# Kernel optimization log

Hardware: AMD Instinct MI355X
Metric: run time of the kernel (lower is better)

The kernel has to match this reference:

```python
import jax, jax.numpy as jnp
import numpy as np

T = 0.07  # temperature from __init__ default


def setup_inputs() -> dict:
    key = jax.random.key(0)
    ks = jax.random.split(key, 5)
    B, D, H, E = 4096, 2048, 2048, 128
    init = lambda k, shp, fan: jax.random.normal(k, shp, dtype=jnp.float32) * (1.0 / np.sqrt(fan))
    return {
        "input1": jax.random.normal(ks[0], (B, D), dtype=jnp.float32),
        "input2": jax.random.normal(ks[1], (B, D), dtype=jnp.float32),
        "W0": init(ks[2], (D, H), D), "b0": jnp.zeros((H,), jnp.float32),
        "W1": init(ks[3], (H, H), H), "b1": jnp.zeros((H,), jnp.float32),
        "W2": init(ks[4], (H, E), H), "b2": jnp.zeros((E,), jnp.float32),
    }


def _mlp(x, W0, b0, W1, b1, W2, b2):
    # Linear -> ReLU -> Linear -> Linear (ReLU only between hidden layers)
    x = jax.nn.relu(x @ W0 + b0)
    x = x @ W1 + b1
    return x @ W2 + b2


def reference(input1, input2, W0, b0, W1, b1, W2, b2):
    B = input1.shape[0]
    e1 = _mlp(input1, W0, b0, W1, b1, W2, b2)
    e2 = _mlp(input2, W0, b0, W1, b1, W2, b2)
    feats = jnp.stack([e1, e2], axis=1)                       # [B, 2, E]
    feats = feats / jnp.linalg.norm(feats, axis=2, keepdims=True)
    # view(N,2,dim).permute(1,0,2).reshape(2N,dim): view0 rows then view1 rows
    f = jnp.concatenate([feats[:, 0], feats[:, 1]], axis=0)   # [2B, E]
    N2 = 2 * B
    sim = (f @ f.T) / T                                        # [2B, 2B]
    idx = jnp.arange(N2)
    pos = sim[idx, (idx + B) % N2]                             # partner view similarity
    # exclude self-similarity (diagonal) from the logsumexp denominator
    sim = jnp.where(jnp.eye(N2, dtype=bool), jnp.float32(-1e9), sim)
    # CE with positive at index 0 of [pos, negatives] == -pos + logsumexp(non-self)
    loss = jnp.mean(jax.nn.logsumexp(sim, axis=1) - pos)
    return loss
```

## Files before the change

kernel.cpp:

```cpp
#include <hip/hip_runtime.h>
#include <stdint.h>

typedef float f32x4 __attribute__((ext_vector_type(4)));
typedef float f32x16 __attribute__((ext_vector_type(16)));
typedef __bf16 bf16x8 __attribute__((ext_vector_type(8)));
typedef unsigned short u16;
typedef unsigned int u32;

#define INVT 14.285714285714286f

__device__ __forceinline__ u16 f2bf(float f) {
  u32 u = __float_as_uint(f);
  u32 r = (u + 0x7fffu + ((u >> 16) & 1u)) >> 16;
  return (u16)r;
}
__device__ __forceinline__ float bf2f(u16 h) { return __uint_as_float(((u32)h) << 16); }

__device__ __forceinline__ void g2l16(const void* g, void* l) {
  auto gp = reinterpret_cast<__attribute__((address_space(1))) uint32_t*>(
      reinterpret_cast<uintptr_t>(g));
  auto lp = reinterpret_cast<__attribute__((address_space(3))) uint32_t*>(
      reinterpret_cast<uintptr_t>(l));
  __builtin_amdgcn_global_load_lds(gp, lp, 16, 0, 0);
}

__global__ __launch_bounds__(256) void k_cvt2(const float* __restrict__ in1,
                                              const float* __restrict__ in2,
                                              u16* __restrict__ out) {
  int i = (blockIdx.x * 256 + threadIdx.x) * 4;
  float4 v;
  if (i < 8388608) v = *(const float4*)(in1 + i);
  else             v = *(const float4*)(in2 + (i - 8388608));
  ushort4 p;
  p.x = f2bf(v.x); p.y = f2bf(v.y); p.z = f2bf(v.z); p.w = f2bf(v.w);
  *(ushort4*)(out + i) = p;
}

__global__ __launch_bounds__(256) void k_transpose2(const float* __restrict__ w0,
                                                    u16* __restrict__ w0t,
                                                    const float* __restrict__ w1,
                                                    u16* __restrict__ w1t) {
  const float* in = blockIdx.z ? w1 : w0;
  u16* out = blockIdx.z ? w1t : w0t;
  const int R = 2048, C = 2048;
  __shared__ float t[64][65];
  const int r0 = blockIdx.y * 64, c0 = blockIdx.x * 64;
#pragma unroll
  for (int p = 0; p < 16; ++p) {
    int idx = p * 256 + threadIdx.x;
    int r = idx >> 6, c = idx & 63;
    t[r][c] = in[(size_t)(r0 + r) * C + (c0 + c)];
  }
  __syncthreads();
#pragma unroll
  for (int p = 0; p < 16; ++p) {
    int idx = p * 256 + threadIdx.x;
    int c = idx >> 6, r = idx & 63;
    out[(size_t)(c0 + c) * R + (r0 + r)] = f2bf(t[r][c]);
  }
}

__global__ __launch_bounds__(256) void k_transpose(const float* __restrict__ in,
                                                   u16* __restrict__ out, int R, int C) {
  __shared__ float t[64][65];
  const int r0 = blockIdx.y * 64, c0 = blockIdx.x * 64;
#pragma unroll
  for (int p = 0; p < 16; ++p) {
    int idx = p * 256 + threadIdx.x;
    int r = idx >> 6, c = idx & 63;
    t[r][c] = in[(size_t)(r0 + r) * C + (c0 + c)];
  }
  __syncthreads();
#pragma unroll
  for (int p = 0; p < 16; ++p) {
    int idx = p * 256 + threadIdx.x;
    int c = idx >> 6, r = idx & 63;
    out[(size_t)(c0 + c) * R + (r0 + r)] = f2bf(t[r][c]);
  }
}

__global__ __launch_bounds__(256, 4) void k_gemm(const u16* __restrict__ A, const u16* __restrict__ Bt,
                                                 const float* __restrict__ bias, u16* __restrict__ C,
                                                 int M, int N, int K, int relu) {
  __shared__ __align__(16) u16 sm[16384];
  const int tid = threadIdx.x;
  const int l = tid & 63, w = tid >> 6;
  const int wm = w >> 1, wn = w & 1;

  const int flat = blockIdx.y * gridDim.x + blockIdx.x;
  const int xcd = flat & 7, slot = flat >> 3;
  const int nb = xcd * 2 + (slot >> 6), mb = slot & 63;
  const int m0 = mb * 128, n0 = nb * 128;

  const int rs = w * 16 + (l >> 2);
  const int kb = ((l & 3) ^ ((rs >> 1) & 3)) * 16;
  const char* gA = (const char*)(A + (size_t)(m0 + rs) * K) + kb;
  const char* gB = (const char*)(Bt + (size_t)(n0 + rs) * K) + kb;
  const size_t radv = (size_t)64 * K * 2;
  char* lbase = (char*)sm + w * 1024 + l * 16;

  auto issue = [&](int kc, int b) {
    char* d = lbase + b * 16384;
    g2l16(gA + kc, d);
    g2l16(gA + radv + kc, d + 4096);
    g2l16(gB + kc, d + 8192);
    g2l16(gB + radv + kc, d + 12288);
  };

  const int rA = wm * 64 + (l & 31);
  const int rB = wn * 64 + (l & 31);
  const int c0 = l >> 5;
  const int sA = (rA >> 1) & 3, sB = (rB >> 1) & 3;

  f32x16 acc[2][2] = {};

  auto compute = [&](int b) {
    const u16* As = sm + b * 8192;
    const u16* Bs = As + 4096;
    bf16x8 af[2][2], bfr[2][2];
#pragma unroll
    for (int t = 0; t < 2; ++t) {
      const int ca = (((t << 1) + c0) ^ sA) * 8;
      const int cb = (((t << 1) + c0) ^ sB) * 8;
#pragma unroll
      for (int fm = 0; fm < 2; ++fm) af[t][fm] = *(const bf16x8*)(As + (rA + fm * 32) * 32 + ca);
#pragma unroll
      for (int fn = 0; fn < 2; ++fn) bfr[t][fn] = *(const bf16x8*)(Bs + (rB + fn * 32) * 32 + cb);
    }
#pragma unroll
    for (int t = 0; t < 2; ++t)
#pragma unroll
      for (int fm = 0; fm < 2; ++fm)
#pragma unroll
        for (int fn = 0; fn < 2; ++fn)
          acc[fm][fn] = __builtin_amdgcn_mfma_f32_32x32x16_bf16(af[t][fm], bfr[t][fn],
                                                                acc[fm][fn], 0, 0, 0);
  };

#define PHASE(BCUR, BNEXT)                                            \
  {                                                                   \
    if (k + 32 < K) {                                                 \
      issue((k + 32) * 2, BNEXT);                                     \
      asm volatile("s_waitcnt vmcnt(4)\ns_barrier" ::: "memory");     \
    } else {                                                          \
      asm volatile("s_waitcnt vmcnt(0)\ns_barrier" ::: "memory");     \
    }                                                                 \
    compute(BCUR);                                                    \
    asm volatile("s_barrier" ::: "memory");                           \
    k += 32;                                                          \
  }

  issue(0, 0);
  int k = 0;
  do { PHASE(0, 1) PHASE(1, 0) } while (k < K);
#undef PHASE

  const int colb = n0 + wn * 64 + (l & 31);
  const int rowb = m0 + wm * 64 + 4 * (l >> 5);
#pragma unroll
  for (int fn = 0; fn < 2; ++fn) {
    const float b = bias[colb + fn * 32];
#pragma unroll
    for (int fm = 0; fm < 2; ++fm)
#pragma unroll
      for (int g = 0; g < 4; ++g)
#pragma unroll
        for (int rr = 0; rr < 4; ++rr) {
          float v = acc[fm][fn][g * 4 + rr] + b;
          if (relu) v = fmaxf(v, 0.0f);
          C[(size_t)(rowb + fm * 32 + g * 8 + rr) * N + colb + fn * 32] = f2bf(v);
        }
  }
}

__global__ __launch_bounds__(256, 4) void k_gemm_sk(const u16* __restrict__ A, const u16* __restrict__ Bt,
                                                    float* __restrict__ Ep, int K, int Ksplit) {
  __shared__ __align__(16) u16 sm[16384];
  const int tid = threadIdx.x;
  const int l = tid & 63, w = tid >> 6;
  const int wm = w >> 1, wn = w & 1;
  const int m0 = blockIdx.y * 128;
  const int split = blockIdx.x;
  const int k0s = split * Ksplit;

  const int rs = w * 16 + (l >> 2);
  const int kb = ((l & 3) ^ ((rs >> 1) & 3)) * 16;
  const char* gA = (const char*)(A + (size_t)(m0 + rs) * K + k0s) + kb;
  const char* gB = (const char*)(Bt + (size_t)rs * K + k0s) + kb;
  const size_t radv = (size_t)64 * K * 2;
  char* lbase = (char*)sm + w * 1024 + l * 16;

  auto issue = [&](int kc, int b) {
    char* d = lbase + b * 16384;
    g2l16(gA + kc, d);
    g2l16(gA + radv + kc, d + 4096);
    g2l16(gB + kc, d + 8192);
    g2l16(gB + radv + kc, d + 12288);
  };

  const int rA = wm * 64 + (l & 31);
  const int rB = wn * 64 + (l & 31);
  const int c0 = l >> 5;
  const int sA = (rA >> 1) & 3, sB = (rB >> 1) & 3;

  f32x16 acc[2][2] = {};

  auto compute = [&](int b) {
    const u16* As = sm + b * 8192;
    const u16* Bs = As + 4096;
    bf16x8 af[2][2], bfr[2][2];
#pragma unroll
    for (int t = 0; t < 2; ++t) {
      const int ca = (((t << 1) + c0) ^ sA) * 8;
      const int cb = (((t << 1) + c0) ^ sB) * 8;
#pragma unroll
      for (int fm = 0; fm < 2; ++fm) af[t][fm] = *(const bf16x8*)(As + (rA + fm * 32) * 32 + ca);
#pragma unroll
      for (int fn = 0; fn < 2; ++fn) bfr[t][fn] = *(const bf16x8*)(Bs + (rB + fn * 32) * 32 + cb);
    }
#pragma unroll
    for (int t = 0; t < 2; ++t)
#pragma unroll
      for (int fm = 0; fm < 2; ++fm)
#pragma unroll
        for (int fn = 0; fn < 2; ++fn)
          acc[fm][fn] = __builtin_amdgcn_mfma_f32_32x32x16_bf16(af[t][fm], bfr[t][fn],
                                                                acc[fm][fn], 0, 0, 0);
  };

#define PHASE(BCUR, BNEXT)                                            \
  {                                                                   \
    if (k + 32 < Ksplit) {                                            \
      issue((k + 32) * 2, BNEXT);                                     \
      asm volatile("s_waitcnt vmcnt(4)\ns_barrier" ::: "memory");     \
    } else {                                                          \
      asm volatile("s_waitcnt vmcnt(0)\ns_barrier" ::: "memory");     \
    }                                                                 \
    compute(BCUR);                                                    \
    asm volatile("s_barrier" ::: "memory");                           \
    k += 32;                                                          \
  }

  issue(0, 0);
  int k = 0;
  do { PHASE(0, 1) PHASE(1, 0) } while (k < Ksplit);
#undef PHASE

  const int colb = wn * 64 + (l & 31);
  const int rowb = wm * 64 + 4 * (l >> 5);
#pragma unroll
  for (int fn = 0; fn < 2; ++fn)
#pragma unroll
    for (int fm = 0; fm < 2; ++fm)
#pragma unroll
      for (int g = 0; g < 4; ++g)
#pragma unroll
        for (int rr = 0; rr < 4; ++rr)
          Ep[((size_t)split * 8192 + m0 + rowb + fm * 32 + g * 8 + rr) * 128 + colb + fn * 32] =
              acc[fm][fn][g * 4 + rr];
}

__global__ __launch_bounds__(256) void k_norm(const float* __restrict__ Ep,
                                              const float* __restrict__ b2, u16* __restrict__ F) {
  const int l = threadIdx.x & 63, w = threadIdx.x >> 6;
  const int row = blockIdx.x * 4 + w;
  const float2* base = (const float2*)Ep + (size_t)row * 64 + l;
  float x = 0.f, y = 0.f;
#pragma unroll
  for (int s = 0; s < 4; ++s) {
    float2 t = base[(size_t)s * (8192 * 64)];
    x += t.x; y += t.y;
  }
  x += b2[l * 2]; y += b2[l * 2 + 1];
  float sq = x * x + y * y;
#pragma unroll
  for (int off = 1; off < 64; off <<= 1) sq += __shfl_xor(sq, off);
  const float inv = 1.0f / sqrtf(sq);
  F[(size_t)row * 128 + l * 2] = f2bf(x * inv);
  F[(size_t)row * 128 + l * 2 + 1] = f2bf(y * inv);
}

__global__ __launch_bounds__(256) void k_sim(const u16* __restrict__ F, float* __restrict__ Sp) {
  __shared__ __align__(16) u16 As[64 * 128];
  const int tid = threadIdx.x;
  const int l = tid & 63, w = tid >> 6;
  const int wm = w >> 1, wn = w & 1;
  const int row0 = blockIdx.y * 64;
  const int chunk = blockIdx.x;

#pragma unroll
  for (int j = 0; j < 4; ++j) {
    const int c = j * 4 + w;
    const int r = c * 4 + (l >> 4);
    const int cb = (l & 15) * 16;
    g2l16((const char*)(F + (size_t)(row0 + r) * 128) + cb, (char*)As + c * 1024 + l * 16);
  }
  asm volatile("s_waitcnt vmcnt(0)" ::: "memory");
  __syncthreads();

  bf16x8 af[2][4];
#pragma unroll
  for (int i = 0; i < 2; ++i)
#pragma unroll
    for (int s = 0; s < 4; ++s)
      af[i][s] = *(const bf16x8*)(As + (wm * 32 + i * 16 + (l & 15)) * 128 + s * 32 + (l >> 4) * 8);

  float runS[2][4] = {};
#pragma unroll 1
  for (int ct = 0; ct < 16; ++ct) {
    const int n0 = chunk * 2048 + ct * 128 + wn * 64;
    f32x4 acc[2][4] = {};
#pragma unroll
    for (int j = 0; j < 4; ++j) {
      const u16* bp = F + (size_t)(n0 + j * 16 + (l & 15)) * 128 + (l >> 4) * 8;
#pragma unroll
      for (int s = 0; s < 4; ++s) {
        bf16x8 bfr = *(const bf16x8*)(bp + s * 32);
        acc[0][j] = __builtin_amdgcn_mfma_f32_16x16x32_bf16(af[0][s], bfr, acc[0][j], 0, 0, 0);
        acc[1][j] = __builtin_amdgcn_mfma_f32_16x16x32_bf16(af[1][s], bfr, acc[1][j], 0, 0, 0);
      }
    }
#pragma unroll
    for (int i = 0; i < 2; ++i) {
      const int rb = row0 + wm * 32 + i * 16 + ((l >> 4) << 2);
#pragma unroll
      for (int r = 0; r < 4; ++r) {
        const int grow = rb + r;
        float sp = 0.f;
#pragma unroll
        for (int j = 0; j < 4; ++j) {
          const int gcol = n0 + j * 16 + (l & 15);
          float v = acc[i][j][r] * INVT;
          v = (gcol == grow) ? -1e30f : v;
          sp += __expf(v - INVT);
        }
        sp += __shfl_xor(sp, 1);
        sp += __shfl_xor(sp, 2);
        sp += __shfl_xor(sp, 4);
        sp += __shfl_xor(sp, 8);
        runS[i][r] += sp;
      }
    }
  }

  __syncthreads();
  float* red = (float*)As;
  if (wn == 0 && (l & 15) == 0) {
#pragma unroll
    for (int i = 0; i < 2; ++i)
#pragma unroll
      for (int r = 0; r < 4; ++r)
        red[wm * 32 + i * 16 + ((l >> 4) << 2) + r] = runS[i][r];
  }
  __syncthreads();
  if (wn == 1 && (l & 15) == 0) {
#pragma unroll
    for (int i = 0; i < 2; ++i)
#pragma unroll
      for (int r = 0; r < 4; ++r) {
        const int rr = wm * 32 + i * 16 + ((l >> 4) << 2) + r;
        Sp[(size_t)chunk * 8192 + row0 + rr] = red[rr] + runS[i][r];
      }
  }
}

__global__ __launch_bounds__(256) void k_combine(const float* __restrict__ Sp,
                                                 const u16* __restrict__ F,
                                                 float* __restrict__ out) {
  const int r = blockIdx.x * 256 + threadIdx.x;
  float S = Sp[r] + Sp[8192 + r] + Sp[2 * 8192 + r] + Sp[3 * 8192 + r];
  const float lse = INVT + logf(S);
  const int par = (r + 4096) & 8191;
  const u16* a = F + (size_t)r * 128;
  const u16* b = F + (size_t)par * 128;
  float dot = 0.f;
#pragma unroll 8
  for (int k = 0; k < 128; ++k) dot = fmaf(bf2f(a[k]), bf2f(b[k]), dot);
  float contrib = lse - dot * INVT;
#pragma unroll
  for (int off = 1; off < 64; off <<= 1) contrib += __shfl_xor(contrib, off);
  if ((threadIdx.x & 63) == 0) atomicAdd(out, contrib * (1.0f / 8192.0f));
}

extern "C" void kernel_launch(void* const* d_in, const int* in_sizes, int n_in,
                              void* d_out, int out_size, void* d_ws, size_t ws_size,
                              hipStream_t stream) {
  const float* input1 = (const float*)d_in[0];
  const float* input2 = (const float*)d_in[1];
  const float* W0 = (const float*)d_in[2];
  const float* b0 = (const float*)d_in[3];
  const float* W1 = (const float*)d_in[4];
  const float* b1 = (const float*)d_in[5];
  const float* W2 = (const float*)d_in[6];
  const float* b2 = (const float*)d_in[7];
  float* out = (float*)d_out;
  char* ws = (char*)d_ws;

  u16* Xb = (u16*)(ws + 0);
  u16* H1 = (u16*)(ws + 33554432);
  u16* W0T = (u16*)(ws + 67108864);
  u16* W1T = (u16*)(ws + 75497472);
  float* Ep = (float*)(ws + 67108864);
  u16* W2T = (u16*)(ws + 83886080);
  u16* Ff = (u16*)(ws + 84410368);
  float* Sp = (float*)(ws + 86507520);
  u16* H2 = Xb;

  hipMemsetAsync(d_out, 0, sizeof(float), stream);
  k_cvt2<<<16384, 256, 0, stream>>>(input1, input2, Xb);
  k_transpose2<<<dim3(32, 32, 2), 256, 0, stream>>>(W0, W0T, W1, W1T);
  k_transpose<<<dim3(2, 32), 256, 0, stream>>>(W2, W2T, 2048, 128);
  k_gemm<<<dim3(16, 64), 256, 0, stream>>>(Xb, W0T, b0, H1, 8192, 2048, 2048, 1);
  k_gemm<<<dim3(16, 64), 256, 0, stream>>>(H1, W1T, b1, H2, 8192, 2048, 2048, 0);
  k_gemm_sk<<<dim3(4, 64), 256, 0, stream>>>(H2, W2T, Ep, 2048, 512);
  k_norm<<<2048, 256, 0, stream>>>(Ep, b2, Ff);
  k_sim<<<dim3(4, 128), 256, 0, stream>>>(Ff, Sp);
  k_combine<<<32, 256, 0, stream>>>(Sp, Ff, out);
}
```

Before: 403.4 us.

## Enlarge GEMM tiles to 256x128 with triple-buffered LDS pipeline

The main GEMMs now use 256x128 block tiles, giving each wave 4x2 MFMA accumulators instead of 2x2 and halving the grid. Both GEMM kernels switch from double buffering with two barriers per k-step to a three-stage LDS ring with one barrier per step, issuing loads two tiles ahead. The larger tiles raise operand reuse per LDS load and cut global traffic per FLOP. In exchange, LDS and register use rise, occupancy drops to two blocks per CU, and the XCD-aware block remapping is removed.

Result: faster. 374.6 us (-7.1%).

```diff
diff --git a/kernel.cpp b/kernel.cpp
--- a/kernel.cpp
+++ b/kernel.cpp
@@ -79,89 +79,81 @@
   }
 }
 
-__global__ __launch_bounds__(256, 4) void k_gemm(const u16* __restrict__ A, const u16* __restrict__ Bt,
+__global__ __launch_bounds__(256, 2) void k_gemm(const u16* __restrict__ A, const u16* __restrict__ Bt,
                                                  const float* __restrict__ bias, u16* __restrict__ C,
                                                  int M, int N, int K, int relu) {
-  __shared__ __align__(16) u16 sm[16384];
+  __shared__ __align__(16) u16 sm[36864];
   const int tid = threadIdx.x;
   const int l = tid & 63, w = tid >> 6;
   const int wm = w >> 1, wn = w & 1;
-
-  const int flat = blockIdx.y * gridDim.x + blockIdx.x;
-  const int xcd = flat & 7, slot = flat >> 3;
-  const int nb = xcd * 2 + (slot >> 6), mb = slot & 63;
-  const int m0 = mb * 128, n0 = nb * 128;
-
-  const int rs = w * 16 + (l >> 2);
-  const int kb = ((l & 3) ^ ((rs >> 1) & 3)) * 16;
-  const char* gA = (const char*)(A + (size_t)(m0 + rs) * K) + kb;
-  const char* gB = (const char*)(Bt + (size_t)(n0 + rs) * K) + kb;
-  const size_t radv = (size_t)64 * K * 2;
-  char* lbase = (char*)sm + w * 1024 + l * 16;
-
-  auto issue = [&](int kc, int b) {
-    char* d = lbase + b * 16384;
-    g2l16(gA + kc, d);
-    g2l16(gA + radv + kc, d + 4096);
-    g2l16(gB + kc, d + 8192);
-    g2l16(gB + radv + kc, d + 12288);
+  const int m0 = blockIdx.y * 256, n0 = blockIdx.x * 128;
+
+  const int kb = ((l & 3) ^ ((l >> 3) & 3)) * 16;
+  const char* gA = (const char*)(A + (size_t)(m0 + w * 64 + (l >> 2)) * K) + kb;
+  const char* gB = (const char*)(Bt + (size_t)(n0 + w * 32 + (l >> 2)) * K) + kb;
+  const size_t chRows = (size_t)16 * K * 2;
+
+  auto issue = [&](int kcB, int stg) {
+    char* base = (char*)sm + stg * 24576;
+    char* dA = base + (w * 4) * 1024 + l * 16;
+    char* dB = base + 16384 + (w * 2) * 1024 + l * 16;
+#pragma unroll
+    for (int j = 0; j < 4; ++j) g2l16(gA + j * chRows + kcB, dA + j * 1024);
+#pragma unroll
+    for (int j = 0; j < 2; ++j) g2l16(gB + j * chRows + kcB, dB + j * 1024);
   };
 
-  const int rA = wm * 64 + (l & 31);
-  const int rB = wn * 64 + (l & 31);
+  const int lm = l & 31;
   const int c0 = l >> 5;
-  const int sA = (rA >> 1) & 3, sB = (rB >> 1) & 3;
-
-  f32x16 acc[2][2] = {};
-
-  auto compute = [&](int b) {
-    const u16* As = sm + b * 8192;
-    const u16* Bs = As + 4096;
-    bf16x8 af[2][2], bfr[2][2];
+  const int sw = (lm >> 1) & 3;
+
+  f32x16 acc[4][2] = {};
+
+  auto compute = [&](int stg) {
+    const u16* As = sm + stg * 12288;
+    const u16* Bs = As + 8192;
 #pragma unroll
     for (int t = 0; t < 2; ++t) {
-      const int ca = (((t << 1) + c0) ^ sA) * 8;
-      const int cb = (((t << 1) + c0) ^ sB) * 8;
-#pragma unroll
-      for (int fm = 0; fm < 2; ++fm) af[t][fm] = *(const bf16x8*)(As + (rA + fm * 32) * 32 + ca);
-#pragma unroll
-      for (int fn = 0; fn < 2; ++fn) bfr[t][fn] = *(const bf16x8*)(Bs + (rB + fn * 32) * 32 + cb);
-    }
-#pragma unroll
-    for (int t = 0; t < 2; ++t)
-#pragma unroll
-      for (int fm = 0; fm < 2; ++fm)
+      const int cc = (((t << 1) + c0) ^ sw) * 8;
+      bf16x8 a4[4], b2[2];
+#pragma unroll
+      for (int fm = 0; fm < 4; ++fm)
+        a4[fm] = *(const bf16x8*)(As + (wm * 128 + fm * 32 + lm) * 32 + cc);
+#pragma unroll
+      for (int fn = 0; fn < 2; ++fn)
+        b2[fn] = *(const bf16x8*)(Bs + (wn * 64 + fn * 32 + lm) * 32 + cc);
+#pragma unroll
+      for (int fm = 0; fm < 4; ++fm)
 #pragma unroll
         for (int fn = 0; fn < 2; ++fn)
-          acc[fm][fn] = __builtin_amdgcn_mfma_f32_32x32x16_bf16(af[t][fm], bfr[t][fn],
+          acc[fm][fn] = __builtin_amdgcn_mfma_f32_32x32x16_bf16(a4[fm], b2[fn],
                                                                 acc[fm][fn], 0, 0, 0);
+    }
   };
 
-#define PHASE(BCUR, BNEXT)                                            \
-  {                                                                   \
-    if (k + 32 < K) {                                                 \
-      issue((k + 32) * 2, BNEXT);                                     \
-      asm volatile("s_waitcnt vmcnt(4)\ns_barrier" ::: "memory");     \
-    } else {                                                          \
-      asm volatile("s_waitcnt vmcnt(0)\ns_barrier" ::: "memory");     \
-    }                                                                 \
-    compute(BCUR);                                                    \
-    asm volatile("s_barrier" ::: "memory");                           \
-    k += 32;                                                          \
-  }
-
+  const int NK = K >> 5;
   issue(0, 0);
-  int k = 0;
-  do { PHASE(0, 1) PHASE(1, 0) } while (k < K);
-#undef PHASE
-
-  const int colb = n0 + wn * 64 + (l & 31);
-  const int rowb = m0 + wm * 64 + 4 * (l >> 5);
+  issue(64, 1);
+  int st = 0;
+  for (int kt = 0; kt < NK; ++kt) {
+    if (kt + 1 < NK) asm volatile("s_waitcnt vmcnt(6)" ::: "memory");
+    else             asm volatile("s_waitcnt vmcnt(0)" ::: "memory");
+    asm volatile("s_barrier" ::: "memory");
+    if (kt + 2 < NK) {
+      int stp = st + 2; if (stp >= 3) stp -= 3;
+      issue((kt + 2) * 64, stp);
+    }
+    compute(st);
+    ++st; if (st == 3) st = 0;
+  }
+
+  const int colb = n0 + wn * 64 + lm;
+  const int rowb = m0 + wm * 128 + 4 * c0;
 #pragma unroll
   for (int fn = 0; fn < 2; ++fn) {
     const float b = bias[colb + fn * 32];
 #pragma unroll
-    for (int fm = 0; fm < 2; ++fm)
+    for (int fm = 0; fm < 4; ++fm)
 #pragma unroll
       for (int g = 0; g < 4; ++g)
 #pragma unroll
@@ -173,9 +165,9 @@
   }
 }
 
-__global__ __launch_bounds__(256, 4) void k_gemm_sk(const u16* __restrict__ A, const u16* __restrict__ Bt,
+__global__ __launch_bounds__(256, 2) void k_gemm_sk(const u16* __restrict__ A, const u16* __restrict__ Bt,
                                                     float* __restrict__ Ep, int K, int Ksplit) {
-  __shared__ __align__(16) u16 sm[16384];
+  __shared__ __align__(16) u16 sm[24576];
   const int tid = threadIdx.x;
   const int l = tid & 63, w = tid >> 6;
   const int wm = w >> 1, wn = w & 1;
@@ -183,71 +175,65 @@
   const int split = blockIdx.x;
   const int k0s = split * Ksplit;
 
-  const int rs = w * 16 + (l >> 2);
-  const int kb = ((l & 3) ^ ((rs >> 1) & 3)) * 16;
-  const char* gA = (const char*)(A + (size_t)(m0 + rs) * K + k0s) + kb;
-  const char* gB = (const char*)(Bt + (size_t)rs * K + k0s) + kb;
+  const int kb = ((l & 3) ^ ((l >> 3) & 3)) * 16;
+  const char* gA = (const char*)(A + (size_t)(m0 + w * 16 + (l >> 2)) * K + k0s) + kb;
+  const char* gB = (const char*)(Bt + (size_t)(w * 16 + (l >> 2)) * K + k0s) + kb;
   const size_t radv = (size_t)64 * K * 2;
-  char* lbase = (char*)sm + w * 1024 + l * 16;
-
-  auto issue = [&](int kc, int b) {
-    char* d = lbase + b * 16384;
-    g2l16(gA + kc, d);
-    g2l16(gA + radv + kc, d + 4096);
-    g2l16(gB + kc, d + 8192);
-    g2l16(gB + radv + kc, d + 12288);
+
+  auto issue = [&](int kcB, int stg) {
+    char* base = (char*)sm + stg * 16384;
+    char* dA = base + w * 1024 + l * 16;
+    char* dB = base + 8192 + w * 1024 + l * 16;
+    g2l16(gA + kcB, dA);
+    g2l16(gA + radv + kcB, dA + 4096);
+    g2l16(gB + kcB, dB);
+    g2l16(gB + radv + kcB, dB + 4096);
   };
 
-  const int rA = wm * 64 + (l & 31);
-  const int rB = wn * 64 + (l & 31);
+  const int lm = l & 31;
   const int c0 = l >> 5;
-  const int sA = (rA >> 1) & 3, sB = (rB >> 1) & 3;
+  const int sw = (lm >> 1) & 3;
 
   f32x16 acc[2][2] = {};
 
-  auto compute = [&](int b) {
-    const u16* As = sm + b * 8192;
+  auto compute = [&](int stg) {
+    const u16* As = sm + stg * 8192;
     const u16* Bs = As + 4096;
-    bf16x8 af[2][2], bfr[2][2];
 #pragma unroll
     for (int t = 0; t < 2; ++t) {
-      const int ca = (((t << 1) + c0) ^ sA) * 8;
-      const int cb = (((t << 1) + c0) ^ sB) * 8;
-#pragma unroll
-      for (int fm = 0; fm < 2; ++fm) af[t][fm] = *(const bf16x8*)(As + (rA + fm * 32) * 32 + ca);
-#pragma unroll
-      for (int fn = 0; fn < 2; ++fn) bfr[t][fn] = *(const bf16x8*)(Bs + (rB + fn * 32) * 32 + cb);
-    }
-#pragma unroll
-    for (int t = 0; t < 2; ++t)
+      const int cc = (((t << 1) + c0) ^ sw) * 8;
+      bf16x8 a2[2], b2[2];
+#pragma unroll
+      for (int fm = 0; fm < 2; ++fm) a2[fm] = *(const bf16x8*)(As + (wm * 64 + fm * 32 + lm) * 32 + cc);
+#pragma unroll
+      for (int fn = 0; fn < 2; ++fn) b2[fn] = *(const bf16x8*)(Bs + (wn * 64 + fn * 32 + lm) * 32 + cc);
 #pragma unroll
       for (int fm = 0; fm < 2; ++fm)
 #pragma unroll
         for (int fn = 0; fn < 2; ++fn)
-          acc[fm][fn] = __builtin_amdgcn_mfma_f32_32x32x16_bf16(af[t][fm], bfr[t][fn],
+          acc[fm][fn] = __builtin_amdgcn_mfma_f32_32x32x16_bf16(a2[fm], b2[fn],
                                                                 acc[fm][fn], 0, 0, 0);
+    }
   };
 
-#define PHASE(BCUR, BNEXT)                                            \
-  {                                                                   \
-    if (k + 32 < Ksplit) {                                            \
-      issue((k + 32) * 2, BNEXT);                                     \
-      asm volatile("s_waitcnt vmcnt(4)\ns_barrier" ::: "memory");     \
-    } else {                                                          \
-      asm volatile("s_waitcnt vmcnt(0)\ns_barrier" ::: "memory");     \
-    }                                                                 \
-    compute(BCUR);                                                    \
-    asm volatile("s_barrier" ::: "memory");                           \
-    k += 32;                                                          \
-  }
-
+  const int NK = Ksplit >> 5;
   issue(0, 0);
-  int k = 0;
-  do { PHASE(0, 1) PHASE(1, 0) } while (k < Ksplit);
-#undef PHASE
-
-  const int colb = wn * 64 + (l & 31);
-  const int rowb = wm * 64 + 4 * (l >> 5);
+  issue(64, 1);
+  int st = 0;
+  for (int kt = 0; kt < NK; ++kt) {
+    if (kt + 1 < NK) asm volatile("s_waitcnt vmcnt(4)" ::: "memory");
+    else             asm volatile("s_waitcnt vmcnt(0)" ::: "memory");
+    asm volatile("s_barrier" ::: "memory");
+    if (kt + 2 < NK) {
+      int stp = st + 2; if (stp >= 3) stp -= 3;
+      issue((kt + 2) * 64, stp);
+    }
+    compute(st);
+    ++st; if (st == 3) st = 0;
+  }
+
+  const int colb = wn * 64 + lm;
+  const int rowb = m0 + wm * 64 + 4 * c0;
 #pragma unroll
   for (int fn = 0; fn < 2; ++fn)
 #pragma unroll
@@ -256,7 +242,7 @@
       for (int g = 0; g < 4; ++g)
 #pragma unroll
         for (int rr = 0; rr < 4; ++rr)
-          Ep[((size_t)split * 8192 + m0 + rowb + fm * 32 + g * 8 + rr) * 128 + colb + fn * 32] =
+          Ep[((size_t)split * 8192 + rowb + fm * 32 + g * 8 + rr) * 128 + colb + fn * 32] =
               acc[fm][fn][g * 4 + rr];
 }
 
@@ -410,8 +396,8 @@
   k_cvt2<<<16384, 256, 0, stream>>>(input1, input2, Xb);
   k_transpose2<<<dim3(32, 32, 2), 256, 0, stream>>>(W0, W0T, W1, W1T);
   k_transpose<<<dim3(2, 32), 256, 0, stream>>>(W2, W2T, 2048, 128);
-  k_gemm<<<dim3(16, 64), 256, 0, stream>>>(Xb, W0T, b0, H1, 8192, 2048, 2048, 1);
-  k_gemm<<<dim3(16, 64), 256, 0, stream>>>(H1, W1T, b1, H2, 8192, 2048, 2048, 0);
+  k_gemm<<<dim3(16, 32), 256, 0, stream>>>(Xb, W0T, b0, H1, 8192, 2048, 2048, 1);
+  k_gemm<<<dim3(16, 32), 256, 0, stream>>>(H1, W1T, b1, H2, 8192, 2048, 2048, 0);
   k_gemm_sk<<<dim3(4, 64), 256, 0, stream>>>(H2, W2T, Ep, 2048, 512);
   k_norm<<<2048, 256, 0, stream>>>(Ep, b2, Ff);
   k_sim<<<dim3(4, 128), 256, 0, stream>>>(Ff, Sp);
```
